# Kernel tuning notes

Measured on AMD Instinct MI355X. Metric: run time of the kernel, lower is better.

Reference implementation:

```python
import jax, jax.numpy as jnp
import numpy as np

E = 512    # len_embeddings
T = 32     # tokennum
H = 256    # hidden_unit
IT = 5     # ICI iterations
B = 4096   # batch
EPS = 1e-6


def setup_inputs() -> dict:
    key = jax.random.key(0)
    k0, k1, k2, k3, k4 = jax.random.split(key, 5)
    x = jax.random.normal(k0, (B, E), dtype=jnp.float32)
    glorot = np.sqrt(2.0 / (E + H)).astype(np.float32)
    w_in = jax.random.normal(k1, (T, E, H), dtype=jnp.float32) * glorot
    w_val = jax.random.normal(k2, (T, E, H), dtype=jnp.float32) * glorot
    # alphas: per-token, per-iteration inhibition strengths (trained; sample nonzero)
    alphas = jax.random.uniform(k3, (T, IT), dtype=jnp.float32) * 0.5
    # scales: per-token output scale (init 1.0, perturb slightly)
    scales = 1.0 + 0.1 * jax.random.normal(k4, (T, H), dtype=jnp.float32)
    gamma = jnp.ones((T, H), dtype=jnp.float32)
    beta = jnp.zeros((T, H), dtype=jnp.float32)
    return {"x": x, "w_in": w_in, "w_val": w_val, "alphas": alphas,
            "scales": scales, "gamma": gamma, "beta": beta}


def reference(x, w_in, w_val, alphas, scales, gamma, beta):
    # batched per-token projection: [B,E] x [T,E,H] -> [B,T,H]
    hidden = jnp.einsum('be,teh->bth', x, w_in)
    # iterative competitive inhibition (fixed small IT loop)
    x_t = jax.nn.relu(hidden)
    for i in range(alphas.shape[1]):
        m = jnp.mean(x_t, axis=-1, keepdims=True)          # [B,T,1]
        a = alphas[:, i][None, :, None]                     # [1,T,1]
        x_t = jax.nn.relu(x_t - a * m)
    sparse_g = scales[None] * x_t                           # [B,T,H]
    # gated value path
    value = jnp.einsum('be,teh->bth', x, w_val)
    s = sparse_g * value
    # per-token LayerNorm over hidden dim, eps=1e-6
    mu = jnp.mean(s, axis=-1, keepdims=True)
    var = jnp.mean((s - mu) ** 2, axis=-1, keepdims=True)
    out = (s - mu) / jnp.sqrt(var + EPS) * gamma[None] + beta[None]
    return out  # [B, T, H]
```

## Files before the change

kernel.cpp:

```cpp
#include <hip/hip_runtime.h>
#include <cstdint>

using u16 = unsigned short;
using u32 = unsigned int;

constexpr int kB  = 4096;
constexpr int kE  = 512;
constexpr int kT  = 32;
constexpr int kH  = 256;
constexpr int kIT = 5;
constexpr float kEPS = 1e-6f;

typedef __attribute__((ext_vector_type(8)))  short short8;
typedef __attribute__((ext_vector_type(16))) float floatx16;
typedef __attribute__((ext_vector_type(8)))  u16   ushort8;

__device__ __forceinline__ u16 f2bf(float f) {
  u32 u = __builtin_bit_cast(u32, f);
  return (u16)((u + 0x7fffu + ((u >> 16) & 1u)) >> 16);
}

__device__ __forceinline__ floatx16 mfma32(short8 a, short8 b, floatx16 c) {
  return __builtin_amdgcn_mfma_f32_32x32x16_bf16(a, b, c, 0, 0, 0);
}

__global__ __launch_bounds__(256) void pack_kernel(
    const float* __restrict__ x, const float* __restrict__ w_in,
    const float* __restrict__ w_val, u16* __restrict__ xp, u16* __restrict__ wp) {
  const int bid = blockIdx.x;
  if (bid < 1024) {
    const int gt = bid * 256 + threadIdx.x;
    const int lane = gt & 63, c = gt >> 6;
    const int mt = c & 1, ks = (c >> 1) & 31, slab = c >> 6;
    const int row = slab * 64 + mt * 32 + (lane & 31);
    const int k   = ks * 16 + (lane >> 5) * 8;
    const float4 f0 = *(const float4*)(x + (size_t)row * kE + k);
    const float4 f1 = *(const float4*)(x + (size_t)row * kE + k + 4);
    ushort8 o;
    o[0] = f2bf(f0.x); o[1] = f2bf(f0.y); o[2] = f2bf(f0.z); o[3] = f2bf(f0.w);
    o[4] = f2bf(f1.x); o[5] = f2bf(f1.y); o[6] = f2bf(f1.z); o[7] = f2bf(f1.w);
    *(ushort8*)(xp + (size_t)c * 512 + lane * 8) = o;
  } else {
    const int gt = (bid - 1024) * 256 + threadIdx.x;
    const int lane = gt & 63, c = gt >> 6;
    const int mat = c & 1, ntile = (c >> 1) & 7, ks = (c >> 4) & 31, t = c >> 9;
    const int n = ntile * 32 + (lane & 31);
    const int k = ks * 16 + (lane >> 5) * 8;
    const float* src = (mat ? w_val : w_in) + (size_t)t * kE * kH;
    ushort8 o;
#pragma unroll
    for (int j = 0; j < 8; ++j) o[j] = f2bf(src[(size_t)(k + j) * kH + n]);
    *(ushort8*)(wp + (size_t)c * 512 + lane * 8) = o;
  }
}

__global__ __launch_bounds__(256) void fused_kernel(
    const u16* __restrict__ xp, const u16* __restrict__ wp,
    const float* __restrict__ alphas, const float* __restrict__ scales,
    const float* __restrict__ gamma, const float* __restrict__ beta,
    float* __restrict__ out) {
  __shared__ __attribute__((aligned(16))) float sAcc[32 * 256];

  const int tid  = threadIdx.x;
  const int wv   = tid >> 6;
  const int lane = tid & 63;
  const int l31  = lane & 31;
  const int h    = lane >> 5;

  const int bid  = blockIdx.x;
  const int xcd  = bid & 7, j_ = bid >> 3;
  const int t    = j_ >> 3;
  const int slab = ((j_ & 7) << 3) | xcd;

  const u16* xpb = xp + (size_t)slab * (32 * 2 * 512) + lane * 8;
  const u16* wpb = wp + (size_t)t * (32 * 16 * 512) + (size_t)(wv * 2) * 1024 + lane * 8;

  floatx16 ai[2][2], av[2][2];
#pragma unroll
  for (int m = 0; m < 2; ++m)
#pragma unroll
    for (int n = 0; n < 2; ++n) { ai[m][n] = (floatx16)0.f; av[m][n] = (floatx16)0.f; }

  short8 A[2][2], BI[2][2], BV[2][2];
  A[0][0]  = *(const short8*)(xpb);
  A[0][1]  = *(const short8*)(xpb + 512);
  BI[0][0] = *(const short8*)(wpb);
  BV[0][0] = *(const short8*)(wpb + 512);
  BI[0][1] = *(const short8*)(wpb + 1024);
  BV[0][1] = *(const short8*)(wpb + 1536);

#pragma unroll
  for (int ks = 0; ks < 32; ++ks) {
    const int cur = ks & 1, nx = cur ^ 1;
    const int kn = (ks < 31) ? ks + 1 : 31;
    A[nx][0]  = *(const short8*)(xpb + kn * 1024);
    A[nx][1]  = *(const short8*)(xpb + kn * 1024 + 512);
    BI[nx][0] = *(const short8*)(wpb + kn * 8192);
    BV[nx][0] = *(const short8*)(wpb + kn * 8192 + 512);
    BI[nx][1] = *(const short8*)(wpb + kn * 8192 + 1024);
    BV[nx][1] = *(const short8*)(wpb + kn * 8192 + 1536);
    ai[0][0] = mfma32(A[cur][0], BI[cur][0], ai[0][0]);
    ai[1][0] = mfma32(A[cur][1], BI[cur][0], ai[1][0]);
    ai[0][1] = mfma32(A[cur][0], BI[cur][1], ai[0][1]);
    ai[1][1] = mfma32(A[cur][1], BI[cur][1], ai[1][1]);
    av[0][0] = mfma32(A[cur][0], BV[cur][0], av[0][0]);
    av[1][0] = mfma32(A[cur][1], BV[cur][0], av[1][0]);
    av[0][1] = mfma32(A[cur][0], BV[cur][1], av[0][1]);
    av[1][1] = mfma32(A[cur][1], BV[cur][1], av[1][1]);
  }

  const float inv_h = 1.0f / kH;
  float al[kIT];
#pragma unroll
  for (int i = 0; i < kIT; ++i) al[i] = alphas[t * kIT + i] * inv_h;

  const int row_r = tid >> 3;
  const int seg   = tid & 7;
  const int r4    = (row_r & 7) << 2;

  for (int mt = 0; mt < 2; ++mt) {
    __syncthreads();
#pragma unroll
    for (int nt = 0; nt < 2; ++nt)
#pragma unroll
      for (int q = 0; q < 16; ++q) {
        const int r   = (q & 3) + 8 * (q >> 2) + 4 * h;
        const int col = wv * 64 + nt * 32 + l31;
        sAcc[r * 256 + (col ^ ((r & 7) << 2))] = ai[mt][nt][q];
      }
    __syncthreads();

    float4 xt[8];
#pragma unroll
    for (int j = 0; j < 8; ++j) {
      xt[j] = *(const float4*)(sAcc + row_r * 256 + seg * 32 + ((4 * j) ^ r4));
#pragma unroll
      for (int i = 0; i < 4; ++i) xt[j][i] = fmaxf(xt[j][i], 0.f);
    }

#pragma unroll
    for (int it = 0; it < kIT; ++it) {
      float4 s4 = xt[0];
#pragma unroll
      for (int j = 1; j < 8; ++j) s4 += xt[j];
      float v = s4.x + s4.y + s4.z + s4.w;
      v += __shfl_xor(v, 1, 8);
      v += __shfl_xor(v, 2, 8);
      v += __shfl_xor(v, 4, 8);
      const float m = al[it] * v;
#pragma unroll
      for (int j = 0; j < 8; ++j)
#pragma unroll
        for (int i = 0; i < 4; ++i) xt[j][i] = fmaxf(xt[j][i] - m, 0.f);
    }

    __syncthreads();
#pragma unroll
    for (int nt = 0; nt < 2; ++nt)
#pragma unroll
      for (int q = 0; q < 16; ++q) {
        const int r   = (q & 3) + 8 * (q >> 2) + 4 * h;
        const int col = wv * 64 + nt * 32 + l31;
        sAcc[r * 256 + (col ^ ((r & 7) << 2))] = av[mt][nt][q];
      }
    __syncthreads();

    float4 res[8];
    float sum = 0.f, ssq = 0.f;
#pragma unroll
    for (int j = 0; j < 8; ++j) {
      const int cb = seg * 32 + ((4 * j) ^ r4);
      const int lc = seg * 32 + 4 * j;
      const float4 a4 = *(const float4*)(sAcc + row_r * 256 + cb);
      const float4 sc = *(const float4*)(scales + t * kH + lc);
      float4 s;
#pragma unroll
      for (int i = 0; i < 4; ++i) {
        s[i] = sc[i] * xt[j][i] * a4[i];
        sum += s[i];
        ssq += s[i] * s[i];
      }
      res[j] = s;
    }
    sum += __shfl_xor(sum, 1, 8);  ssq += __shfl_xor(ssq, 1, 8);
    sum += __shfl_xor(sum, 2, 8);  ssq += __shfl_xor(ssq, 2, 8);
    sum += __shfl_xor(sum, 4, 8);  ssq += __shfl_xor(ssq, 4, 8);
    const float mu  = sum * inv_h;
    const float var = ssq * inv_h - mu * mu;
    const float rs  = rsqrtf(var + kEPS);

#pragma unroll
    for (int j = 0; j < 8; ++j) {
      const int cb = seg * 32 + ((4 * j) ^ r4);
      const int lc = seg * 32 + 4 * j;
      const float4 g4 = *(const float4*)(gamma + t * kH + lc);
      const float4 b4 = *(const float4*)(beta + t * kH + lc);
      float4 o;
#pragma unroll
      for (int i = 0; i < 4; ++i) o[i] = (res[j][i] - mu) * rs * g4[i] + b4[i];
      *(float4*)(sAcc + row_r * 256 + cb) = o;
    }
    __syncthreads();

#pragma unroll
    for (int r8 = 0; r8 < 8; ++r8) {
      const int rr = wv * 8 + r8;
      const int rb = (rr & 7) << 2;
      const float4 v = *(const float4*)(sAcc + rr * 256 + ((4 * lane) ^ rb));
      *(float4*)(out + (size_t)(slab * 64 + mt * 32 + rr) * (kT * kH) + t * kH + 4 * lane) = v;
    }
  }
}

extern "C" void kernel_launch(void* const* d_in, const int* in_sizes, int n_in,
                              void* d_out, int out_size, void* d_ws, size_t ws_size,
                              hipStream_t stream) {
  const float* x      = (const float*)d_in[0];
  const float* w_in   = (const float*)d_in[1];
  const float* w_val  = (const float*)d_in[2];
  const float* alphas = (const float*)d_in[3];
  const float* scales = (const float*)d_in[4];
  const float* gamma  = (const float*)d_in[5];
  const float* beta   = (const float*)d_in[6];
  float* out = (float*)d_out;

  u16* xp = (u16*)d_ws;
  u16* wp = xp + (size_t)64 * 32 * 2 * 512;

  pack_kernel<<<5120, 256, 0, stream>>>(x, w_in, w_val, xp, wp);
  fused_kernel<<<kT * (kB / 64), 256, 0, stream>>>(xp, wp, alphas, scales,
                                                   gamma, beta, out);
}
```

Measured before the change: 357.4 us.

## Transpose weights through LDS tiles in pack kernel and use nontemporal loads/stores

The weight-packing path now stages 64x64 fp32 weight tiles in shared memory with coalesced float4 loads and then emits bf16 MFMA fragments from LDS. Before, each thread did strided scalar global reads down the E dimension. The grid for that path shrinks to match the tile count. Separately, the x and weight reads and the final output stores use nontemporal hints to reduce cache pollution. The cost is an extra LDS round-trip and a barrier per pack block.

```diff
diff --git a/kernel.cpp b/kernel.cpp
--- a/kernel.cpp
+++ b/kernel.cpp
@@ -14,6 +14,7 @@
 typedef __attribute__((ext_vector_type(8)))  short short8;
 typedef __attribute__((ext_vector_type(16))) float floatx16;
 typedef __attribute__((ext_vector_type(8)))  u16   ushort8;
+typedef __attribute__((ext_vector_type(4)))  float floatv4;
 
 __device__ __forceinline__ u16 f2bf(float f) {
   u32 u = __builtin_bit_cast(u32, f);
@@ -22,6 +23,14 @@
 
 __device__ __forceinline__ floatx16 mfma32(short8 a, short8 b, floatx16 c) {
   return __builtin_amdgcn_mfma_f32_32x32x16_bf16(a, b, c, 0, 0, 0);
+}
+
+__device__ __forceinline__ float4 ntload4(const float* p) {
+  floatv4 v = __builtin_nontemporal_load((const floatv4*)p);
+  return __builtin_bit_cast(float4, v);
+}
+__device__ __forceinline__ void ntstore4(float* p, float4 v) {
+  __builtin_nontemporal_store(__builtin_bit_cast(floatv4, v), (floatv4*)p);
 }
 
 __global__ __launch_bounds__(256) void pack_kernel(
@@ -34,23 +43,43 @@
     const int mt = c & 1, ks = (c >> 1) & 31, slab = c >> 6;
     const int row = slab * 64 + mt * 32 + (lane & 31);
     const int k   = ks * 16 + (lane >> 5) * 8;
-    const float4 f0 = *(const float4*)(x + (size_t)row * kE + k);
-    const float4 f1 = *(const float4*)(x + (size_t)row * kE + k + 4);
+    const float4 f0 = ntload4(x + (size_t)row * kE + k);
+    const float4 f1 = ntload4(x + (size_t)row * kE + k + 4);
     ushort8 o;
     o[0] = f2bf(f0.x); o[1] = f2bf(f0.y); o[2] = f2bf(f0.z); o[3] = f2bf(f0.w);
     o[4] = f2bf(f1.x); o[5] = f2bf(f1.y); o[6] = f2bf(f1.z); o[7] = f2bf(f1.w);
     *(ushort8*)(xp + (size_t)c * 512 + lane * 8) = o;
   } else {
-    const int gt = (bid - 1024) * 256 + threadIdx.x;
-    const int lane = gt & 63, c = gt >> 6;
-    const int mat = c & 1, ntile = (c >> 1) & 7, ks = (c >> 4) & 31, t = c >> 9;
-    const int n = ntile * 32 + (lane & 31);
-    const int k = ks * 16 + (lane >> 5) * 8;
-    const float* src = (mat ? w_val : w_in) + (size_t)t * kE * kH;
-    ushort8 o;
-#pragma unroll
-    for (int j = 0; j < 8; ++j) o[j] = f2bf(src[(size_t)(k + j) * kH + n]);
-    *(ushort8*)(wp + (size_t)c * 512 + lane * 8) = o;
+    __shared__ float tile[64 * 68];
+    const int wb   = bid - 1024;
+    const int tl   = wb & 31;
+    const int et   = tl >> 2;
+    const int ht   = tl & 3;
+    const int tm   = wb >> 5;
+    const int t    = tm >> 1, mat = tm & 1;
+    const int tid  = threadIdx.x;
+    const float* src = (mat ? w_val : w_in) + (size_t)t * kE * kH +
+                       (size_t)(et * 64) * kH + ht * 64;
+    const int lrow = tid >> 4, lc4 = (tid & 15) * 4;
+#pragma unroll
+    for (int p = 0; p < 4; ++p) {
+      const int e = lrow + p * 16;
+      const float4 v = ntload4(src + (size_t)e * kH + lc4);
+      tile[e * 68 + lc4 + 0] = v.x; tile[e * 68 + lc4 + 1] = v.y;
+      tile[e * 68 + lc4 + 2] = v.z; tile[e * 68 + lc4 + 3] = v.w;
+    }
+    __syncthreads();
+    const int ks_l = tid >> 6, lane = tid & 63;
+    const int kloc = ks_l * 16 + (lane >> 5) * 8;
+#pragma unroll
+    for (int nt_l = 0; nt_l < 2; ++nt_l) {
+      const int nloc = nt_l * 32 + (lane & 31);
+      ushort8 o;
+#pragma unroll
+      for (int j = 0; j < 8; ++j) o[j] = f2bf(tile[(kloc + j) * 68 + nloc]);
+      const int c = t * 512 + (et * 4 + ks_l) * 16 + (ht * 2 + nt_l) * 2 + mat;
+      *(ushort8*)(wp + (size_t)c * 512 + lane * 8) = o;
+    }
   }
 }
 
@@ -207,7 +236,7 @@
       const int rr = wv * 8 + r8;
       const int rb = (rr & 7) << 2;
       const float4 v = *(const float4*)(sAcc + rr * 256 + ((4 * lane) ^ rb));
-      *(float4*)(out + (size_t)(slab * 64 + mt * 32 + rr) * (kT * kH) + t * kH + 4 * lane) = v;
+      ntstore4(out + (size_t)(slab * 64 + mt * 32 + rr) * (kT * kH) + t * kH + 4 * lane, v);
     }
   }
 }
@@ -227,7 +256,7 @@
   u16* xp = (u16*)d_ws;
   u16* wp = xp + (size_t)64 * 32 * 2 * 512;
 
-  pack_kernel<<<5120, 256, 0, stream>>>(x, w_in, w_val, xp, wp);
+  pack_kernel<<<1024 + 2048, 256, 0, stream>>>(x, w_in, w_val, xp, wp);
   fused_kernel<<<kT * (kB / 64), 256, 0, stream>>>(xp, wp, alphas, scales,
                                                    gamma, beta, out);
 }
```

Result: no change. 360.6 us (+0.9%).
